# Kernel optimization log

Measured on AMD Instinct MI355X. Metric: run time of the kernel, lower is better.

Reference implementation:

```python
import jax, jax.numpy as jnp
import numpy as np

N, E = 50000, 800000
IN_C, HID, OUT_C, HEADS = 768, 64, 8, 8
NEG_SLOPE = 0.2
BN_EPS = 1e-5


def _bn(x, g, b, m, v):
    # BatchNorm1d in eval mode with running stats
    return (x - m) * jax.lax.rsqrt(v + BN_EPS) * g + b


def _gat_conv(x, W, att_src, att_dst, bias, src, dst, n):
    H, C = att_src.shape
    xw = (x @ W).reshape(n, H, C)                      # [N,H,C]
    a_src = jnp.sum(xw * att_src, axis=-1)             # [N,H]
    a_dst = jnp.sum(xw * att_dst, axis=-1)             # [N,H]
    alpha = jax.nn.leaky_relu(a_src[src] + a_dst[dst], NEG_SLOPE)  # [E',H]
    amax = jax.ops.segment_max(alpha, dst, num_segments=n)          # [N,H]
    ex = jnp.exp(alpha - amax[dst])
    denom = jax.ops.segment_sum(ex, dst, num_segments=n)            # [N,H]
    coef = ex / denom[dst]                                          # [E',H]
    out = jax.ops.segment_sum(xw[src] * coef[:, :, None], dst, num_segments=n)
    return out.reshape(n, H * C) + bias


def setup_inputs() -> dict:
    key = jax.random.key(0)
    ks = jax.random.split(key, 24)
    d = {}
    d['x'] = jax.random.normal(ks[0], (N, IN_C), dtype=jnp.float32)
    d['edge_index'] = jax.random.randint(ks[1], (2, E), 0, N, dtype=jnp.int32)
    d['proj_W'] = jax.random.normal(ks[2], (IN_C, HID), dtype=jnp.float32) * (IN_C ** -0.5)
    d['proj_b'] = jnp.zeros((HID,), jnp.float32)
    for i, kb in zip((1, 2, 3), (ks[3], ks[4], ks[5])):
        k1, k2 = jax.random.split(kb)
        d[f'bn{i}_g'] = jnp.ones((HID,), jnp.float32)
        d[f'bn{i}_b'] = jnp.zeros((HID,), jnp.float32)
        d[f'bn{i}_m'] = jax.random.normal(k1, (HID,), dtype=jnp.float32) * 0.1
        d[f'bn{i}_v'] = jax.random.uniform(k2, (HID,), dtype=jnp.float32, minval=0.5, maxval=1.5)
    C1 = HID // HEADS
    d['W1'] = jax.random.normal(ks[6], (HID, HEADS * C1), dtype=jnp.float32) * (HID ** -0.5)
    d['att_src1'] = jax.random.normal(ks[7], (HEADS, C1), dtype=jnp.float32) * 0.1
    d['att_dst1'] = jax.random.normal(ks[8], (HEADS, C1), dtype=jnp.float32) * 0.1
    d['b1'] = jnp.zeros((HEADS * C1,), jnp.float32)
    d['W2'] = jax.random.normal(ks[9], (HID, HID), dtype=jnp.float32) * (HID ** -0.5)
    d['att_src2'] = jax.random.normal(ks[10], (1, HID), dtype=jnp.float32) * 0.1
    d['att_dst2'] = jax.random.normal(ks[11], (1, HID), dtype=jnp.float32) * 0.1
    d['b2'] = jnp.zeros((HID,), jnp.float32)
    d['cls_W'] = jax.random.normal(ks[12], (HID, OUT_C), dtype=jnp.float32) * (HID ** -0.5)
    d['cls_b'] = jnp.zeros((OUT_C,), jnp.float32)
    return d


def reference(x, edge_index, proj_W, proj_b,
              bn1_g, bn1_b, bn1_m, bn1_v,
              W1, att_src1, att_dst1, b1,
              bn2_g, bn2_b, bn2_m, bn2_v,
              W2, att_src2, att_dst2, b2,
              bn3_g, bn3_b, bn3_m, bn3_v,
              cls_W, cls_b):
    n = x.shape[0]
    # add self-loops (PyG GATConv default)
    loop = jnp.arange(n, dtype=edge_index.dtype)
    src = jnp.concatenate([edge_index[0], loop])
    dst = jnp.concatenate([edge_index[1], loop])

    h = x @ proj_W + proj_b
    h = jax.nn.elu(_bn(h, bn1_g, bn1_b, bn1_m, bn1_v))
    identity = h
    h = _gat_conv(h, W1, att_src1, att_dst1, b1, src, dst, n)
    h = jax.nn.elu(_bn(h, bn2_g, bn2_b, bn2_m, bn2_v) + identity)
    identity = h
    h = _gat_conv(h, W2, att_src2, att_dst2, b2, src, dst, n)
    h = jax.nn.elu(_bn(h, bn3_g, bn3_b, bn3_m, bn3_v) + identity)
    return h @ cls_W + cls_b
```

## Files before the change

kernel.cpp:

```cpp
#include <hip/hip_runtime.h>

typedef __bf16 bf16;
typedef __attribute__((ext_vector_type(8))) __bf16 bf16x8;
typedef __attribute__((ext_vector_type(4))) float f32x4;

#define LSTR 40
#define BN_EPS 1e-5f

__global__ __launch_bounds__(256) void k_transpose(
        const float* __restrict__ W0, const float* __restrict__ W1, const float* __restrict__ W2,
        bf16* __restrict__ Wt0, bf16* __restrict__ Wt1, bf16* __restrict__ Wt2)
{
    int i = blockIdx.x*256 + threadIdx.x;
    if (i < 768*64)            { int k = i>>6, n = i&63;                   Wt0[n*768+k] = (bf16)W0[i]; }
    else if (i < 768*64+4096)  { int j = i-768*64;      int k=j>>6,n=j&63; Wt1[n*64+k]  = (bf16)W1[j]; }
    else if (i < 768*64+8192)  { int j = i-768*64-4096; int k=j>>6,n=j&63; Wt2[n*64+k]  = (bf16)W2[j]; }
}

template<int MODE>
__global__ __launch_bounds__(256) void k_gemm64(
        const float* __restrict__ A, const bf16* __restrict__ Bt, int M, int K,
        const float* __restrict__ pb, const float* __restrict__ g, const float* __restrict__ bb,
        const float* __restrict__ mm, const float* __restrict__ vv,
        float* __restrict__ outF, bf16* __restrict__ outB)
{
    __shared__ bf16 xs[64*LSTR];
    __shared__ bf16 bs[64*LSTR];
    __shared__ float sC[64], cC[64];

    int t = threadIdx.x;
    int w = t >> 6, lane = t & 63;
    int q = lane >> 4, l16 = lane & 15;
    int row0 = blockIdx.x * 64;
    int sRow = t >> 2, sK = (t & 3) * 8;

    f32x4 acc[4];
    #pragma unroll
    for (int i = 0; i < 4; ++i) { acc[i][0]=0.f; acc[i][1]=0.f; acc[i][2]=0.f; acc[i][3]=0.f; }

    for (int k0 = 0; k0 < K; k0 += 32) {
        bf16x8 xv;
        #pragma unroll
        for (int i = 0; i < 8; ++i) xv[i] = (bf16)0.f;
        int gr = row0 + sRow;
        if (gr < M) {
            const float* ap = A + (size_t)gr*K + k0 + sK;
            float4 f0 = *(const float4*)ap;
            float4 f1 = *(const float4*)(ap + 4);
            xv[0]=(bf16)f0.x; xv[1]=(bf16)f0.y; xv[2]=(bf16)f0.z; xv[3]=(bf16)f0.w;
            xv[4]=(bf16)f1.x; xv[5]=(bf16)f1.y; xv[6]=(bf16)f1.z; xv[7]=(bf16)f1.w;
        }
        *(bf16x8*)(xs + sRow*LSTR + sK) = xv;
        bf16x8 bv = *(const bf16x8*)(Bt + (size_t)sRow*K + k0 + sK);
        *(bf16x8*)(bs + sRow*LSTR + sK) = bv;
        __syncthreads();

        bf16x8 af = *(bf16x8*)(xs + (w*16 + l16)*LSTR + q*8);
        #pragma unroll
        for (int tt = 0; tt < 4; ++tt) {
            bf16x8 bfr = *(bf16x8*)(bs + (tt*16 + l16)*LSTR + q*8);
            acc[tt] = __builtin_amdgcn_mfma_f32_16x16x32_bf16(af, bfr, acc[tt], 0, 0, 0);
        }
        __syncthreads();
    }

    if constexpr (MODE == 0) {
        if (t < 64) {
            float s = rsqrtf(vv[t] + BN_EPS) * g[t];
            sC[t] = s;
            cC[t] = (pb[t] - mm[t]) * s + bb[t];
        }
        __syncthreads();
    }
    #pragma unroll
    for (int tt = 0; tt < 4; ++tt) {
        int col = tt*16 + l16;
        #pragma unroll
        for (int r = 0; r < 4; ++r) {
            int row = row0 + w*16 + q*4 + r;
            if (row < M) {
                float val = acc[tt][r];
                if constexpr (MODE == 0) {
                    val = val * sC[col] + cC[col];
                    val = val > 0.f ? val : __expf(val) - 1.f;
                    outF[(size_t)row*64 + col] = val;
                } else {
                    outB[(size_t)row*64 + col] = (bf16)val;
                }
            }
        }
    }
}

__global__ __launch_bounds__(256) void k_init_counts(int* cnt, int n) {
    int i = blockIdx.x*256 + threadIdx.x;
    if (i < n) cnt[i] = 1;
}
__global__ __launch_bounds__(256) void k_count(const int* __restrict__ dst, int E, int* cnt) {
    int i = blockIdx.x*256 + threadIdx.x;
    if (i < E) atomicAdd(&cnt[dst[i]], 1);
}
__global__ __launch_bounds__(256) void k_scan_block(const int* __restrict__ cnt,
        int* __restrict__ rp, int* __restrict__ bsum, int n) {
    __shared__ int s[256];
    int t = threadIdx.x, v = blockIdx.x*256 + t;
    int x = (v < n) ? cnt[v] : 0;
    s[t] = x; __syncthreads();
    for (int off = 1; off < 256; off <<= 1) {
        int y = (t >= off) ? s[t-off] : 0;
        __syncthreads();
        s[t] += y;
        __syncthreads();
    }
    if (v < n) rp[v+1] = s[t];
    if (t == 255) bsum[blockIdx.x] = s[255];
}
__global__ __launch_bounds__(256) void k_scan_bsum(int* bsum, int nb) {
    __shared__ int s[256];
    int t = threadIdx.x;
    int x = (t < nb) ? bsum[t] : 0;
    s[t] = x; __syncthreads();
    for (int off = 1; off < 256; off <<= 1) {
        int y = (t >= off) ? s[t-off] : 0;
        __syncthreads();
        s[t] += y;
        __syncthreads();
    }
    if (t < nb) bsum[t] = s[t] - x;
}
__global__ __launch_bounds__(256) void k_finalize(int* __restrict__ rp, const int* __restrict__ bsum,
        const int* __restrict__ cnt, int* __restrict__ cursor, int n) {
    int v = blockIdx.x*256 + threadIdx.x;
    if (v < n) {
        int val = rp[v+1] + bsum[v >> 8];
        rp[v+1] = val;
        cursor[v] = val - cnt[v];
        if (v == 0) rp[0] = 0;
    }
}
__global__ __launch_bounds__(256) void k_scatter(const int* __restrict__ src, const int* __restrict__ dst,
        int E, int n, int* __restrict__ cursor, int* __restrict__ in_src) {
    int i = blockIdx.x*256 + threadIdx.x;
    if (i < E) {
        int pos = atomicAdd(&cursor[dst[i]], 1);
        in_src[pos] = src[i];
    } else if (i < E + n) {
        int v = i - E;
        int pos = atomicAdd(&cursor[v], 1);
        in_src[pos] = v;
    }
}

template<int H>
__global__ __launch_bounds__(256) void k_compute_a(const bf16* __restrict__ xwb,
        const float* __restrict__ att_s, const float* __restrict__ att_d,
        float* __restrict__ a_src, float* __restrict__ a_dst, int n)
{
    int wv = (blockIdx.x*256 + threadIdx.x) >> 6;
    int lane = threadIdx.x & 63;
    if (wv >= n) return;
    float x = (float)xwb[(size_t)wv*64 + lane];
    float ps = x * att_s[lane];
    float pd = x * att_d[lane];
    const int C = 64 / H;
    #pragma unroll
    for (int off = 1; off < C; off <<= 1) {
        ps += __shfl_xor(ps, off);
        pd += __shfl_xor(pd, off);
    }
    if ((lane & (C-1)) == 0) {
        int h = lane / C;
        a_src[wv*H + h] = ps;
        a_dst[wv*H + h] = pd;
    }
}

template<int H, bool CLS>
__global__ __launch_bounds__(256) void k_gat_agg(const bf16* __restrict__ xwb,
        const float* __restrict__ a_src, const float* __restrict__ a_dst,
        const int* __restrict__ rp, const int* __restrict__ in_src,
        const float* __restrict__ bias,
        const float* __restrict__ g, const float* __restrict__ bb,
        const float* __restrict__ mm, const float* __restrict__ vv,
        const float* __restrict__ resid, float* __restrict__ out,
        const float* __restrict__ clsW, const float* __restrict__ clsb, int n)
{
    int wv = (blockIdx.x*256 + threadIdx.x) >> 6;
    int lane = threadIdx.x & 63;
    if (wv >= n) return;
    int h = (H == 8) ? (lane >> 3) : 0;
    float adst = a_dst[wv*H + h];
    int beg = rp[wv], end = rp[wv+1];
    float acc = 0.f, den = 0.f;
    int e = beg;
    for (; e + 4 <= end; e += 4) {
        int u0 = in_src[e+0], u1 = in_src[e+1], u2 = in_src[e+2], u3 = in_src[e+3];
        float s0 = a_src[u0*H + h], s1 = a_src[u1*H + h];
        float s2 = a_src[u2*H + h], s3 = a_src[u3*H + h];
        float x0 = (float)xwb[(size_t)u0*64 + lane];
        float x1 = (float)xwb[(size_t)u1*64 + lane];
        float x2 = (float)xwb[(size_t)u2*64 + lane];
        float x3 = (float)xwb[(size_t)u3*64 + lane];
        float a0 = s0 + adst; a0 = (a0 > 0.f) ? a0 : 0.2f*a0; float e0 = __expf(a0);
        float a1 = s1 + adst; a1 = (a1 > 0.f) ? a1 : 0.2f*a1; float e1 = __expf(a1);
        float a2 = s2 + adst; a2 = (a2 > 0.f) ? a2 : 0.2f*a2; float e2 = __expf(a2);
        float a3 = s3 + adst; a3 = (a3 > 0.f) ? a3 : 0.2f*a3; float e3 = __expf(a3);
        acc += e0*x0 + e1*x1 + e2*x2 + e3*x3;
        den += e0 + e1 + e2 + e3;
    }
    for (; e < end; ++e) {
        int u = in_src[e];
        float al = a_src[u*H + h] + adst;
        al = (al > 0.f) ? al : 0.2f*al;
        float ex = __expf(al);
        acc += ex * (float)xwb[(size_t)u*64 + lane];
        den += ex;
    }
    float val = acc/den + bias[lane];
    float sc = rsqrtf(vv[lane] + BN_EPS) * g[lane];
    val = (val - mm[lane]) * sc + bb[lane];
    val += resid[(size_t)wv*64 + lane];
    val = (val > 0.f) ? val : __expf(val) - 1.f;

    if constexpr (!CLS) {
        out[(size_t)wv*64 + lane] = val;
    } else {
        float keep = 0.f;
        #pragma unroll
        for (int o = 0; o < 8; ++o) {
            float p = val * clsW[lane*8 + o];
            #pragma unroll
            for (int off = 1; off < 64; off <<= 1) p += __shfl_xor(p, off);
            if (lane == o) keep = p + clsb[o];
        }
        if (lane < 8) out[(size_t)wv*8 + lane] = keep;
    }
}

extern "C" void kernel_launch(void* const* d_in, const int* in_sizes, int n_in,
                              void* d_out, int out_size, void* d_ws, size_t ws_size,
                              hipStream_t stream)
{
    const float* x      = (const float*)d_in[0];
    const int*   ei     = (const int*)  d_in[1];
    const float* proj_W = (const float*)d_in[2];
    const float* proj_b = (const float*)d_in[3];
    const float* bn1_g  = (const float*)d_in[4];
    const float* bn1_b  = (const float*)d_in[5];
    const float* bn1_m  = (const float*)d_in[6];
    const float* bn1_v  = (const float*)d_in[7];
    const float* bn2_g  = (const float*)d_in[8];
    const float* bn2_b  = (const float*)d_in[9];
    const float* bn2_m  = (const float*)d_in[10];
    const float* bn2_v  = (const float*)d_in[11];
    const float* bn3_g  = (const float*)d_in[12];
    const float* bn3_b  = (const float*)d_in[13];
    const float* bn3_m  = (const float*)d_in[14];
    const float* bn3_v  = (const float*)d_in[15];
    const float* W1     = (const float*)d_in[16];
    const float* att_s1 = (const float*)d_in[17];
    const float* att_d1 = (const float*)d_in[18];
    const float* b1     = (const float*)d_in[19];
    const float* W2     = (const float*)d_in[20];
    const float* att_s2 = (const float*)d_in[21];
    const float* att_d2 = (const float*)d_in[22];
    const float* b2     = (const float*)d_in[23];
    const float* cls_W  = (const float*)d_in[24];
    const float* cls_b  = (const float*)d_in[25];

    const int N = in_sizes[0] / 768;
    const int E = in_sizes[1] / 2;
    const int* srce = ei;
    const int* dste = ei + E;

    char* p = (char*)d_ws;
    auto carve = [&](size_t bytes) -> void* {
        void* r = (void*)p;
        p += (bytes + 255) & ~(size_t)255;
        return r;
    };
    bf16*  Wt0    = (bf16*) carve((size_t)64*768*2);
    bf16*  Wt1    = (bf16*) carve((size_t)64*64*2);
    bf16*  Wt2    = (bf16*) carve((size_t)64*64*2);
    float* h0     = (float*)carve((size_t)N*64*4);
    float* h1     = (float*)carve((size_t)N*64*4);
    bf16*  xwb    = (bf16*) carve((size_t)N*64*2);
    float* a_s    = (float*)carve((size_t)N*8*4);
    float* a_d    = (float*)carve((size_t)N*8*4);
    int*   cnt    = (int*)  carve((size_t)N*4);
    int*   rp     = (int*)  carve((size_t)(N+1)*4);
    int*   cursor = (int*)  carve((size_t)N*4);
    int*   bsum   = (int*)  carve(1024);
    int*   in_src = (int*)  carve((size_t)(E+N)*4);

    const int nb = (N + 255) / 256;

    k_transpose<<<(768*64 + 8192 + 255)/256, 256, 0, stream>>>(proj_W, W1, W2, Wt0, Wt1, Wt2);

    k_init_counts<<<nb, 256, 0, stream>>>(cnt, N);
    k_count<<<(E + 255)/256, 256, 0, stream>>>(dste, E, cnt);
    k_scan_block<<<nb, 256, 0, stream>>>(cnt, rp, bsum, N);
    k_scan_bsum<<<1, 256, 0, stream>>>(bsum, nb);
    k_finalize<<<nb, 256, 0, stream>>>(rp, bsum, cnt, cursor, N);
    k_scatter<<<(E + N + 255)/256, 256, 0, stream>>>(srce, dste, E, N, cursor, in_src);

    k_gemm64<0><<<(N + 63)/64, 256, 0, stream>>>(x, Wt0, N, 768,
            proj_b, bn1_g, bn1_b, bn1_m, bn1_v, h0, nullptr);

    k_gemm64<1><<<(N + 63)/64, 256, 0, stream>>>(h0, Wt1, N, 64,
            nullptr, nullptr, nullptr, nullptr, nullptr, nullptr, xwb);
    k_compute_a<8><<<(N + 3)/4, 256, 0, stream>>>(xwb, att_s1, att_d1, a_s, a_d, N);
    k_gat_agg<8, false><<<(N + 3)/4, 256, 0, stream>>>(xwb, a_s, a_d, rp, in_src,
            b1, bn2_g, bn2_b, bn2_m, bn2_v, h0, h1, nullptr, nullptr, N);

    k_gemm64<1><<<(N + 63)/64, 256, 0, stream>>>(h1, Wt2, N, 64,
            nullptr, nullptr, nullptr, nullptr, nullptr, nullptr, xwb);
    k_compute_a<1><<<(N + 3)/4, 256, 0, stream>>>(xwb, att_s2, att_d2, a_s, a_d, N);
    k_gat_agg<1, true><<<(N + 3)/4, 256, 0, stream>>>(xwb, a_s, a_d, rp, in_src,
            b2, bn3_g, bn3_b, bn3_m, bn3_v, h1, (float*)d_out, cls_W, cls_b, N);
}
```

Before: 532.1 us.

## Fuse attention-logit computation into GEMM epilogue, store activations as bf16, prefetch tiles

Moves the per-node attention score computation (a_src/a_dst) into the epilogue of the small GEMMs, so two compute_a kernels and their re-read of xw go away. Intermediate activations h0/h1 are now stored as bf16 instead of fp32, halving their write and read traffic in the GEMMs and in the residual reads. The GEMM main loop also software-prefetches the next A/B tile into registers before the MFMA step. The cost is extra bf16 rounding on the residual path and the second-layer inputs, and attention logits are now taken from fp32 accumulators rather than from bf16-rounded xw.

Measured after the change: 507.4 us. 4.6% less time.

```diff
diff --git a/kernel.cpp b/kernel.cpp
--- a/kernel.cpp
+++ b/kernel.cpp
@@ -17,12 +17,14 @@
     else if (i < 768*64+8192)  { int j = i-768*64-4096; int k=j>>6,n=j&63; Wt2[n*64+k]  = (bf16)W2[j]; }
 }
 
-template<int MODE>
+template<int MODE, bool ABF, int H>
 __global__ __launch_bounds__(256) void k_gemm64(
-        const float* __restrict__ A, const bf16* __restrict__ Bt, int M, int K,
+        const void* __restrict__ Av, const bf16* __restrict__ Bt, int M, int K,
         const float* __restrict__ pb, const float* __restrict__ g, const float* __restrict__ bb,
         const float* __restrict__ mm, const float* __restrict__ vv,
-        float* __restrict__ outF, bf16* __restrict__ outB)
+        bf16* __restrict__ outB,
+        float* __restrict__ a_s, float* __restrict__ a_d,
+        const float* __restrict__ att_s, const float* __restrict__ att_d)
 {
     __shared__ bf16 xs[64*LSTR];
     __shared__ bf16 bs[64*LSTR];
@@ -34,27 +36,43 @@
     int row0 = blockIdx.x * 64;
     int sRow = t >> 2, sK = (t & 3) * 8;
 
+    auto loadA = [&](int k0) -> bf16x8 {
+        bf16x8 xv;
+        #pragma unroll
+        for (int i = 0; i < 8; ++i) xv[i] = (bf16)0.f;
+        int gr = row0 + sRow;
+        if (gr < M) {
+            if constexpr (ABF) {
+                xv = *(const bf16x8*)((const bf16*)Av + (size_t)gr*K + k0 + sK);
+            } else {
+                const float* ap = (const float*)Av + (size_t)gr*K + k0 + sK;
+                float4 f0 = *(const float4*)ap;
+                float4 f1 = *(const float4*)(ap + 4);
+                xv[0]=(bf16)f0.x; xv[1]=(bf16)f0.y; xv[2]=(bf16)f0.z; xv[3]=(bf16)f0.w;
+                xv[4]=(bf16)f1.x; xv[5]=(bf16)f1.y; xv[6]=(bf16)f1.z; xv[7]=(bf16)f1.w;
+            }
+        }
+        return xv;
+    };
+    auto loadB = [&](int k0) -> bf16x8 {
+        return *(const bf16x8*)(Bt + (size_t)sRow*K + k0 + sK);
+    };
+
     f32x4 acc[4];
     #pragma unroll
     for (int i = 0; i < 4; ++i) { acc[i][0]=0.f; acc[i][1]=0.f; acc[i][2]=0.f; acc[i][3]=0.f; }
 
+    bf16x8 xv = loadA(0);
+    bf16x8 bv = loadB(0);
+
     for (int k0 = 0; k0 < K; k0 += 32) {
-        bf16x8 xv;
-        #pragma unroll
-        for (int i = 0; i < 8; ++i) xv[i] = (bf16)0.f;
-        int gr = row0 + sRow;
-        if (gr < M) {
-            const float* ap = A + (size_t)gr*K + k0 + sK;
-            float4 f0 = *(const float4*)ap;
-            float4 f1 = *(const float4*)(ap + 4);
-            xv[0]=(bf16)f0.x; xv[1]=(bf16)f0.y; xv[2]=(bf16)f0.z; xv[3]=(bf16)f0.w;
-            xv[4]=(bf16)f1.x; xv[5]=(bf16)f1.y; xv[6]=(bf16)f1.z; xv[7]=(bf16)f1.w;
-        }
         *(bf16x8*)(xs + sRow*LSTR + sK) = xv;
-        bf16x8 bv = *(const bf16x8*)(Bt + (size_t)sRow*K + k0 + sK);
         *(bf16x8*)(bs + sRow*LSTR + sK) = bv;
         __syncthreads();
-
+        if (k0 + 32 < K) {
+            xv = loadA(k0 + 32);
+            bv = loadB(k0 + 32);
+        }
         bf16x8 af = *(bf16x8*)(xs + (w*16 + l16)*LSTR + q*8);
         #pragma unroll
         for (int tt = 0; tt < 4; ++tt) {
@@ -72,6 +90,7 @@
         }
         __syncthreads();
     }
+
     #pragma unroll
     for (int tt = 0; tt < 4; ++tt) {
         int col = tt*16 + l16;
@@ -83,9 +102,53 @@
                 if constexpr (MODE == 0) {
                     val = val * sC[col] + cC[col];
                     val = val > 0.f ? val : __expf(val) - 1.f;
-                    outF[(size_t)row*64 + col] = val;
-                } else {
-                    outB[(size_t)row*64 + col] = (bf16)val;
+                }
+                outB[(size_t)row*64 + col] = (bf16)val;
+            }
+        }
+    }
+
+    if constexpr (MODE == 1) {
+        #pragma unroll
+        for (int r = 0; r < 4; ++r) {
+            int row = row0 + w*16 + q*4 + r;
+            if constexpr (H == 1) {
+                float ps = 0.f, pd = 0.f;
+                #pragma unroll
+                for (int tt = 0; tt < 4; ++tt) {
+                    int col = tt*16 + l16;
+                    ps += acc[tt][r] * att_s[col];
+                    pd += acc[tt][r] * att_d[col];
+                }
+                #pragma unroll
+                for (int off = 1; off < 16; off <<= 1) {
+                    ps += __shfl_xor(ps, off);
+                    pd += __shfl_xor(pd, off);
+                }
+                if (l16 == 0 && row < M) { a_s[row] = ps; a_d[row] = pd; }
+            } else {
+                float ps[4], pd[4];
+                #pragma unroll
+                for (int tt = 0; tt < 4; ++tt) {
+                    int col = tt*16 + l16;
+                    ps[tt] = acc[tt][r] * att_s[col];
+                    pd[tt] = acc[tt][r] * att_d[col];
+                }
+                #pragma unroll
+                for (int off = 1; off < 8; off <<= 1) {
+                    #pragma unroll
+                    for (int tt = 0; tt < 4; ++tt) {
+                        ps[tt] += __shfl_xor(ps[tt], off);
+                        pd[tt] += __shfl_xor(pd[tt], off);
+                    }
+                }
+                if ((l16 & 7) == 0 && row < M) {
+                    int hb = l16 >> 3;
+                    #pragma unroll
+                    for (int tt = 0; tt < 4; ++tt) {
+                        a_s[row*8 + 2*tt + hb] = ps[tt];
+                        a_d[row*8 + 2*tt + hb] = pd[tt];
+                    }
                 }
             }
         }
@@ -151,30 +214,6 @@
     }
 }
 
-template<int H>
-__global__ __launch_bounds__(256) void k_compute_a(const bf16* __restrict__ xwb,
-        const float* __restrict__ att_s, const float* __restrict__ att_d,
-        float* __restrict__ a_src, float* __restrict__ a_dst, int n)
-{
-    int wv = (blockIdx.x*256 + threadIdx.x) >> 6;
-    int lane = threadIdx.x & 63;
-    if (wv >= n) return;
-    float x = (float)xwb[(size_t)wv*64 + lane];
-    float ps = x * att_s[lane];
-    float pd = x * att_d[lane];
-    const int C = 64 / H;
-    #pragma unroll
-    for (int off = 1; off < C; off <<= 1) {
-        ps += __shfl_xor(ps, off);
-        pd += __shfl_xor(pd, off);
-    }
-    if ((lane & (C-1)) == 0) {
-        int h = lane / C;
-        a_src[wv*H + h] = ps;
-        a_dst[wv*H + h] = pd;
-    }
-}
-
 template<int H, bool CLS>
 __global__ __launch_bounds__(256) void k_gat_agg(const bf16* __restrict__ xwb,
         const float* __restrict__ a_src, const float* __restrict__ a_dst,
@@ -182,7 +221,7 @@
         const float* __restrict__ bias,
         const float* __restrict__ g, const float* __restrict__ bb,
         const float* __restrict__ mm, const float* __restrict__ vv,
-        const float* __restrict__ resid, float* __restrict__ out,
+        const bf16* __restrict__ resid, bf16* __restrict__ outB, float* __restrict__ outF,
         const float* __restrict__ clsW, const float* __restrict__ clsb, int n)
 {
     int wv = (blockIdx.x*256 + threadIdx.x) >> 6;
@@ -219,11 +258,11 @@
     float val = acc/den + bias[lane];
     float sc = rsqrtf(vv[lane] + BN_EPS) * g[lane];
     val = (val - mm[lane]) * sc + bb[lane];
-    val += resid[(size_t)wv*64 + lane];
+    val += (float)resid[(size_t)wv*64 + lane];
     val = (val > 0.f) ? val : __expf(val) - 1.f;
 
     if constexpr (!CLS) {
-        out[(size_t)wv*64 + lane] = val;
+        outB[(size_t)wv*64 + lane] = (bf16)val;
     } else {
         float keep = 0.f;
         #pragma unroll
@@ -233,7 +272,7 @@
             for (int off = 1; off < 64; off <<= 1) p += __shfl_xor(p, off);
             if (lane == o) keep = p + clsb[o];
         }
-        if (lane < 8) out[(size_t)wv*8 + lane] = keep;
+        if (lane < 8) outF[(size_t)wv*8 + lane] = keep;
     }
 }
 
@@ -282,8 +321,8 @@
     bf16*  Wt0    = (bf16*) carve((size_t)64*768*2);
     bf16*  Wt1    = (bf16*) carve((size_t)64*64*2);
     bf16*  Wt2    = (bf16*) carve((size_t)64*64*2);
-    float* h0     = (float*)carve((size_t)N*64*4);
-    float* h1     = (float*)carve((size_t)N*64*4);
+    bf16*  h0b    = (bf16*) carve((size_t)N*64*2);
+    bf16*  h1b    = (bf16*) carve((size_t)N*64*2);
     bf16*  xwb    = (bf16*) carve((size_t)N*64*2);
     float* a_s    = (float*)carve((size_t)N*8*4);
     float* a_d    = (float*)carve((size_t)N*8*4);
@@ -304,18 +343,16 @@
     k_finalize<<<nb, 256, 0, stream>>>(rp, bsum, cnt, cursor, N);
     k_scatter<<<(E + N + 255)/256, 256, 0, stream>>>(srce, dste, E, N, cursor, in_src);
 
-    k_gemm64<0><<<(N + 63)/64, 256, 0, stream>>>(x, Wt0, N, 768,
-            proj_b, bn1_g, bn1_b, bn1_m, bn1_v, h0, nullptr);
-
-    k_gemm64<1><<<(N + 63)/64, 256, 0, stream>>>(h0, Wt1, N, 64,
-            nullptr, nullptr, nullptr, nullptr, nullptr, nullptr, xwb);
-    k_compute_a<8><<<(N + 3)/4, 256, 0, stream>>>(xwb, att_s1, att_d1, a_s, a_d, N);
+    k_gemm64<0, false, 1><<<(N + 63)/64, 256, 0, stream>>>(x, Wt0, N, 768,
+            proj_b, bn1_g, bn1_b, bn1_m, bn1_v, h0b, nullptr, nullptr, nullptr, nullptr);
+
+    k_gemm64<1, true, 8><<<(N + 63)/64, 256, 0, stream>>>(h0b, Wt1, N, 64,
+            nullptr, nullptr, nullptr, nullptr, nullptr, xwb, a_s, a_d, att_s1, att_d1);
     k_gat_agg<8, false><<<(N + 3)/4, 256, 0, stream>>>(xwb, a_s, a_d, rp, in_src,
-            b1, bn2_g, bn2_b, bn2_m, bn2_v, h0, h1, nullptr, nullptr, N);
-
-    k_gemm64<1><<<(N + 63)/64, 256, 0, stream>>>(h1, Wt2, N, 64,
-            nullptr, nullptr, nullptr, nullptr, nullptr, nullptr, xwb);
-    k_compute_a<1><<<(N + 3)/4, 256, 0, stream>>>(xwb, att_s2, att_d2, a_s, a_d, N);
+            b1, bn2_g, bn2_b, bn2_m, bn2_v, h0b, h1b, nullptr, nullptr, nullptr, N);
+
+    k_gemm64<1, true, 1><<<(N + 63)/64, 256, 0, stream>>>(h1b, Wt2, N, 64,
+            nullptr, nullptr, nullptr, nullptr, nullptr, xwb, a_s, a_d, att_s2, att_d2);
     k_gat_agg<1, true><<<(N + 3)/4, 256, 0, stream>>>(xwb, a_s, a_d, rp, in_src,
-            b2, bn3_g, bn3_b, bn3_m, bn3_v, h1, (float*)d_out, cls_W, cls_b, N);
-}
+            b2, bn3_g, bn3_b, bn3_m, bn3_v, h1b, nullptr, (float*)d_out, cls_W, cls_b, N);
+}
```
